# Performance work log

Measured on AMD Instinct MI355X. Metric: run time of the kernel, lower is better.

Reference implementation:

```python
import jax, jax.numpy as jnp
import numpy as np

DIM = 1024
BLOCK = 64
N_BLOCKS = DIM // BLOCK
N = 65536
INIT_SCALE = 0.01


def setup_inputs() -> dict:
    key = jax.random.key(0)
    k1, k2 = jax.random.split(key)
    x = jax.random.normal(k1, (N, DIM), dtype=jnp.float32)
    skew_params = jax.random.normal(k2, (N_BLOCKS, BLOCK, BLOCK), dtype=jnp.float32) * INIT_SCALE
    perm = jnp.asarray(np.random.default_rng(0).permutation(DIM), dtype=jnp.int64)
    return {"x": x, "skew_params": skew_params, "perm": perm}


def reference(x, skew_params, perm):
    # Skew-symmetrize each block: A = P - P^T, shape [K, b, b]
    A = skew_params - jnp.swapaxes(skew_params, -1, -2)
    # Per-block orthogonal matrices via matrix exponential, [K, b, b]
    B = jax.vmap(jax.scipy.linalg.expm)(A)
    # Block-diagonal matmul without materializing the dense [dim, dim] matrix:
    # x @ block_diag(B_0..B_{K-1}) == batched per-block matmul on reshaped x.
    xb = x.reshape(x.shape[0], N_BLOCKS, BLOCK)          # [N, K, b]
    yb = jnp.einsum("nkb,kbc->nkc", xb, B)               # [N, K, b]
    y = yb.reshape(x.shape[0], DIM)                      # [N, dim]
    # Shuffle: column permutation
    return y[:, perm]
```

## Files before the change

### kernel.cpp

```cpp
#include <hip/hip_runtime.h>

#define DIM           1024
#define BLK           64
#define NB            16
#define RT            16
#define MAIN_THREADS  1024
#define NWG           256
#define TPW           16
#define P68           68
#define BFRAG_STRIDE  512

typedef float  f32x4  __attribute__((ext_vector_type(4)));
typedef unsigned uintx2 __attribute__((ext_vector_type(2)));
typedef short  bf16x8 __attribute__((ext_vector_type(8)));

static __device__ __forceinline__ ushort f2bf(float f) {
    union { float f; unsigned u; } v; v.f = f;
    unsigned r = v.u + 0x7fffu + ((v.u >> 16) & 1u);
    return (ushort)(r >> 16);
}
static __device__ __forceinline__ float bfhi2f(unsigned hi_bits) {
    union { unsigned u; float f; } v; v.u = hi_bits & 0xffff0000u; return v.f;
}
static __device__ __forceinline__ float bflo2f(unsigned lo_bits) {
    union { unsigned u; float f; } v; v.u = lo_bits << 16; return v.f;
}

#define WAITL()   asm volatile("s_waitcnt lgkmcnt(0)" ::: "memory")
#define SBAR()    __builtin_amdgcn_s_barrier()

__global__ __launch_bounds__(512) void expm_kernel(
        const float* __restrict__ skew, ushort* __restrict__ Btl,
        const int* __restrict__ praw, int* __restrict__ pinv) {
    __shared__ float Asm[BLK][P68];
    __shared__ float Tb[2][BLK][P68];
    __shared__ float Rm[BLK][P68];
    const int tid = threadIdx.x;

    if (blockIdx.x == NB) {
        __shared__ int zc;
        if (tid == 0) zc = 0;
        __syncthreads();
        int local = 0;
        for (int i = tid; i < DIM; i += 512)
            if (praw[i] == 0) local++;
        if (local) atomicAdd(&zc, local);
        __syncthreads();
        const bool is64 = (zc > 100);
        const long long* p64 = (const long long*)praw;
        for (int i = tid; i < DIM; i += 512) {
            const int v = is64 ? (int)p64[i] : praw[i];
            pinv[v] = i;
        }
        return;
    }

    const int k = blockIdx.x;
    const float* P = skew + (size_t)k * (BLK * BLK);

    for (int e = tid; e < BLK * BLK; e += 512) {
        const int i = e >> 6, j = e & 63;
        const float a = P[i * BLK + j] - P[j * BLK + i];
        Asm[i][j]   = a;
        Tb[0][i][j] = a;
        Rm[i][j]    = a + (i == j ? 1.0f : 0.0f);
    }
    __syncthreads();

    const int i0 = (tid >> 4) * 2;
    const int j0 = (tid & 15) * 4;

    for (int n = 2; n <= 7; ++n) {
        const float invn = 1.0f / (float)n;
        const float (*Tc)[P68] = Tb[n & 1];
        float       (*Tn)[P68] = Tb[1 - (n & 1)];
        f32x4 acc0 = {0.f, 0.f, 0.f, 0.f}, acc1 = {0.f, 0.f, 0.f, 0.f};
        for (int b = 0; b < BLK; ++b) {
            const f32x4 av = *(const f32x4*)&Asm[b][j0];
            acc0 += Tc[i0][b]     * av;
            acc1 += Tc[i0 + 1][b] * av;
        }
        acc0 *= invn; acc1 *= invn;
        *(f32x4*)&Tn[i0][j0]     = acc0;
        *(f32x4*)&Tn[i0 + 1][j0] = acc1;
        f32x4 r0 = *(const f32x4*)&Rm[i0][j0];     r0 += acc0; *(f32x4*)&Rm[i0][j0]     = r0;
        f32x4 r1 = *(const f32x4*)&Rm[i0 + 1][j0]; r1 += acc1; *(f32x4*)&Rm[i0 + 1][j0] = r1;
        __syncthreads();
    }

    for (int e = tid; e < BLK * BLK; e += 512) {
        const int b = e >> 6, c = e & 63;
        const int n = c >> 4, m = c & 15;
        const int h = b >> 5, g = (b >> 3) & 3, j = b & 7;
        const size_t idx = (size_t)((k * 4 + n) * 2 + h) * BFRAG_STRIDE
                         + g * 128 + m * 8 + j;
        Btl[idx] = (ushort)f2bf(Rm[b][c]);
    }
}

__global__ __launch_bounds__(MAIN_THREADS) void gsl_main_kernel(
        const float* __restrict__ x, const ushort* __restrict__ Btl,
        const int* __restrict__ pinv, float* __restrict__ out) {
    __shared__ ushort ybuf[2][RT * DIM];

    const int tid  = threadIdx.x;
    const int lane = tid & 63;
    const int w    = tid >> 6;
    const int g    = lane >> 4;
    const int m16  = lane & 15;

    bf16x8 bfr[4][2];
#pragma unroll
    for (int n = 0; n < 4; ++n)
#pragma unroll
        for (int h = 0; h < 2; ++h)
            bfr[n][h] = *(const bf16x8*)(Btl +
                (size_t)((w * 4 + n) * 2 + h) * BFRAG_STRIDE + lane * 8);

    int jb[4];
#pragma unroll
    for (int n = 0; n < 4; ++n)
        jb[n] = pinv[w * 64 + n * 16 + m16] * 2;

    const int tile0 = blockIdx.x * TPW;
    const float* xw = x + w * 64 + g * 8;

    const int hl   = lane >> 5;
    const int q32  = lane & 31;
    const int ebase = hl * 512 + q32 * 4;

    f32x4 a0, a1, a2, a3;
    {
        const float* xp = xw + (size_t)(tile0 * RT + m16) * DIM;
        a0 = *(const f32x4*)(xp);      a1 = *(const f32x4*)(xp + 4);
        a2 = *(const f32x4*)(xp + 32); a3 = *(const f32x4*)(xp + 36);
    }

    for (int it = 0; it < TPW; ++it) {
        char* const yc = (char*)ybuf[it & 1];

        bf16x8 alo, ahi;
        alo[0] = f2bf(a0[0]); alo[1] = f2bf(a0[1]); alo[2] = f2bf(a0[2]); alo[3] = f2bf(a0[3]);
        alo[4] = f2bf(a1[0]); alo[5] = f2bf(a1[1]); alo[6] = f2bf(a1[2]); alo[7] = f2bf(a1[3]);
        ahi[0] = f2bf(a2[0]); ahi[1] = f2bf(a2[1]); ahi[2] = f2bf(a2[2]); ahi[3] = f2bf(a2[3]);
        ahi[4] = f2bf(a3[0]); ahi[5] = f2bf(a3[1]); ahi[6] = f2bf(a3[2]); ahi[7] = f2bf(a3[3]);

        if (it + 1 < TPW) {
            const float* xp = xw + (size_t)((tile0 + it + 1) * RT + m16) * DIM;
            a0 = *(const f32x4*)(xp);      a1 = *(const f32x4*)(xp + 4);
            a2 = *(const f32x4*)(xp + 32); a3 = *(const f32x4*)(xp + 36);
        }

        f32x4 acc[4];
#pragma unroll
        for (int n = 0; n < 4; ++n) acc[n] = (f32x4){0.f, 0.f, 0.f, 0.f};
#pragma unroll
        for (int n = 0; n < 4; ++n)
            acc[n] = __builtin_amdgcn_mfma_f32_16x16x32_bf16(alo, bfr[n][0], acc[n], 0, 0, 0);
#pragma unroll
        for (int n = 0; n < 4; ++n)
            acc[n] = __builtin_amdgcn_mfma_f32_16x16x32_bf16(ahi, bfr[n][1], acc[n], 0, 0, 0);

#pragma unroll
        for (int n = 0; n < 4; ++n)
#pragma unroll
            for (int i = 0; i < 4; ++i)
                *(ushort*)(yc + (4 * g + i) * 2048 + jb[n]) = f2bf(acc[n][i]);

        if (it) {
            const char* yp = (const char*)ybuf[(it & 1) ^ 1] + w * 2048;
            float* orow = out + (size_t)((tile0 + it - 1) * RT + w) * DIM;
#pragma unroll
            for (int i = 0; i < 4; ++i) {
                const int e = ebase + i * 128;
                const uintx2 u = *(const uintx2*)(yp + e * 2);
                f32x4 v;
                v[0] = bflo2f(u[0]); v[1] = bfhi2f(u[0]);
                v[2] = bflo2f(u[1]); v[3] = bfhi2f(u[1]);
                *(f32x4*)(orow + e) = v;
            }
        }

        WAITL(); SBAR();
    }

    {
        const char* yp = (const char*)ybuf[(TPW - 1) & 1] + w * 2048;
        float* orow = out + (size_t)((tile0 + TPW - 1) * RT + w) * DIM;
#pragma unroll
        for (int i = 0; i < 4; ++i) {
            const int e = ebase + i * 128;
            const uintx2 u = *(const uintx2*)(yp + e * 2);
            f32x4 v;
            v[0] = bflo2f(u[0]); v[1] = bfhi2f(u[0]);
            v[2] = bflo2f(u[1]); v[3] = bfhi2f(u[1]);
            *(f32x4*)(orow + e) = v;
        }
    }
}

extern "C" void kernel_launch(void* const* d_in, const int* in_sizes, int n_in,
                              void* d_out, int out_size, void* d_ws, size_t ws_size,
                              hipStream_t stream) {
    const float* x    = (const float*)d_in[0];
    const float* skew = (const float*)d_in[1];
    const int*   perm = (const int*)d_in[2];
    float* out = (float*)d_out;

    ushort* Btl  = (ushort*)d_ws;
    int*    pinv = (int*)((char*)d_ws + (size_t)NB * BLK * BLK * sizeof(ushort));

    expm_kernel<<<NB + 1, 512, 0, stream>>>(skew, Btl, perm, pinv);
    gsl_main_kernel<<<NWG, MAIN_THREADS, 0, stream>>>(x, Btl, pinv, out);
}
```

Measured before the change: 132.2 us.

## Replace persistent 1024-thread pipelined loop with small one-tile workgroups

The main kernel drops the persistent design, where 256 workgroups of 1024 threads each looped over 16 row tiles with double-buffered LDS and a software-prefetched x load. It now launches 4096 workgroups of 256 threads, one 16-row tile each, with every wave handling four column blocks and reloading their B fragments and inverse-permutation indices. The fp32-to-bf16 conversion of x switches to the packed v_cvt_pk_bf16_f32 instruction. The aim is higher occupancy (launch bounds ask for 5 blocks per SIMD) and letting the hardware overlap tiles across workgroups instead of relying on manual prefetch, at the cost of more redundant B and pinv loads.

```diff
diff --git a/kernel.cpp b/kernel.cpp
--- a/kernel.cpp
+++ b/kernel.cpp
@@ -4,14 +4,14 @@
 #define BLK           64
 #define NB            16
 #define RT            16
-#define MAIN_THREADS  1024
-#define NWG           256
-#define TPW           16
+#define MAIN_THREADS  256
+#define NWG           4096
 #define P68           68
 #define BFRAG_STRIDE  512
 
 typedef float  f32x4  __attribute__((ext_vector_type(4)));
 typedef unsigned uintx2 __attribute__((ext_vector_type(2)));
+typedef int    i32x4  __attribute__((ext_vector_type(4)));
 typedef short  bf16x8 __attribute__((ext_vector_type(8)));
 
 static __device__ __forceinline__ ushort f2bf(float f) {
@@ -25,9 +25,11 @@
 static __device__ __forceinline__ float bflo2f(unsigned lo_bits) {
     union { unsigned u; float f; } v; v.u = lo_bits << 16; return v.f;
 }
-
-#define WAITL()   asm volatile("s_waitcnt lgkmcnt(0)" ::: "memory")
-#define SBAR()    __builtin_amdgcn_s_barrier()
+static __device__ __forceinline__ unsigned cvt_pk(float lo, float hi) {
+    unsigned r;
+    asm("v_cvt_pk_bf16_f32 %0, %1, %2" : "=v"(r) : "v"(lo), "v"(hi));
+    return r;
+}
 
 __global__ __launch_bounds__(512) void expm_kernel(
         const float* __restrict__ skew, ushort* __restrict__ Btl,
@@ -98,58 +100,48 @@
     }
 }
 
-__global__ __launch_bounds__(MAIN_THREADS) void gsl_main_kernel(
+__global__ __launch_bounds__(MAIN_THREADS, 5) void gsl_main_kernel(
         const float* __restrict__ x, const ushort* __restrict__ Btl,
         const int* __restrict__ pinv, float* __restrict__ out) {
-    __shared__ ushort ybuf[2][RT * DIM];
+    __shared__ ushort ybuf[RT * DIM];
 
     const int tid  = threadIdx.x;
     const int lane = tid & 63;
     const int w    = tid >> 6;
     const int g    = lane >> 4;
     const int m16  = lane & 15;
+    const size_t r0 = (size_t)blockIdx.x * RT;
+    char* const yB = (char*)ybuf;
 
-    bf16x8 bfr[4][2];
+    for (int b = 0; b < 4; ++b) {
+        const int k = w + 4 * b;
+
+        int jb[4];
 #pragma unroll
-    for (int n = 0; n < 4; ++n)
+        for (int n = 0; n < 4; ++n)
+            jb[n] = pinv[k * 64 + n * 16 + m16] * 2;
+
+        bf16x8 bfr[4][2];
 #pragma unroll
-        for (int h = 0; h < 2; ++h)
-            bfr[n][h] = *(const bf16x8*)(Btl +
-                (size_t)((w * 4 + n) * 2 + h) * BFRAG_STRIDE + lane * 8);
+        for (int n = 0; n < 4; ++n)
+#pragma unroll
+            for (int h = 0; h < 2; ++h)
+                bfr[n][h] = *(const bf16x8*)(Btl +
+                    (size_t)((k * 4 + n) * 2 + h) * BFRAG_STRIDE + lane * 8);
 
-    int jb[4];
-#pragma unroll
-    for (int n = 0; n < 4; ++n)
-        jb[n] = pinv[w * 64 + n * 16 + m16] * 2;
+        const float* xp = x + (r0 + m16) * DIM + k * 64 + g * 8;
+        const f32x4 a0 = *(const f32x4*)(xp);
+        const f32x4 a1 = *(const f32x4*)(xp + 4);
+        const f32x4 a2 = *(const f32x4*)(xp + 32);
+        const f32x4 a3 = *(const f32x4*)(xp + 36);
 
-    const int tile0 = blockIdx.x * TPW;
-    const float* xw = x + w * 64 + g * 8;
-
-    const int hl   = lane >> 5;
-    const int q32  = lane & 31;
-    const int ebase = hl * 512 + q32 * 4;
-
-    f32x4 a0, a1, a2, a3;
-    {
-        const float* xp = xw + (size_t)(tile0 * RT + m16) * DIM;
-        a0 = *(const f32x4*)(xp);      a1 = *(const f32x4*)(xp + 4);
-        a2 = *(const f32x4*)(xp + 32); a3 = *(const f32x4*)(xp + 36);
-    }
-
-    for (int it = 0; it < TPW; ++it) {
-        char* const yc = (char*)ybuf[it & 1];
-
-        bf16x8 alo, ahi;
-        alo[0] = f2bf(a0[0]); alo[1] = f2bf(a0[1]); alo[2] = f2bf(a0[2]); alo[3] = f2bf(a0[3]);
-        alo[4] = f2bf(a1[0]); alo[5] = f2bf(a1[1]); alo[6] = f2bf(a1[2]); alo[7] = f2bf(a1[3]);
-        ahi[0] = f2bf(a2[0]); ahi[1] = f2bf(a2[1]); ahi[2] = f2bf(a2[2]); ahi[3] = f2bf(a2[3]);
-        ahi[4] = f2bf(a3[0]); ahi[5] = f2bf(a3[1]); ahi[6] = f2bf(a3[2]); ahi[7] = f2bf(a3[3]);
-
-        if (it + 1 < TPW) {
-            const float* xp = xw + (size_t)((tile0 + it + 1) * RT + m16) * DIM;
-            a0 = *(const f32x4*)(xp);      a1 = *(const f32x4*)(xp + 4);
-            a2 = *(const f32x4*)(xp + 32); a3 = *(const f32x4*)(xp + 36);
-        }
+        i32x4 plo, phi;
+        plo[0] = cvt_pk(a0[0], a0[1]); plo[1] = cvt_pk(a0[2], a0[3]);
+        plo[2] = cvt_pk(a1[0], a1[1]); plo[3] = cvt_pk(a1[2], a1[3]);
+        phi[0] = cvt_pk(a2[0], a2[1]); phi[1] = cvt_pk(a2[2], a2[3]);
+        phi[2] = cvt_pk(a3[0], a3[1]); phi[3] = cvt_pk(a3[2], a3[3]);
+        const bf16x8 alo = __builtin_bit_cast(bf16x8, plo);
+        const bf16x8 ahi = __builtin_bit_cast(bf16x8, phi);
 
         f32x4 acc[4];
 #pragma unroll
@@ -165,31 +157,21 @@
         for (int n = 0; n < 4; ++n)
 #pragma unroll
             for (int i = 0; i < 4; ++i)
-                *(ushort*)(yc + (4 * g + i) * 2048 + jb[n]) = f2bf(acc[n][i]);
-
-        if (it) {
-            const char* yp = (const char*)ybuf[(it & 1) ^ 1] + w * 2048;
-            float* orow = out + (size_t)((tile0 + it - 1) * RT + w) * DIM;
-#pragma unroll
-            for (int i = 0; i < 4; ++i) {
-                const int e = ebase + i * 128;
-                const uintx2 u = *(const uintx2*)(yp + e * 2);
-                f32x4 v;
-                v[0] = bflo2f(u[0]); v[1] = bfhi2f(u[0]);
-                v[2] = bflo2f(u[1]); v[3] = bfhi2f(u[1]);
-                *(f32x4*)(orow + e) = v;
-            }
-        }
-
-        WAITL(); SBAR();
+                *(ushort*)(yB + (4 * g + i) * 2048 + jb[n]) = f2bf(acc[n][i]);
     }
 
-    {
-        const char* yp = (const char*)ybuf[(TPW - 1) & 1] + w * 2048;
-        float* orow = out + (size_t)((tile0 + TPW - 1) * RT + w) * DIM;
+    __syncthreads();
+
+    const int h32  = lane >> 5;
+    const int q32  = lane & 31;
 #pragma unroll
-        for (int i = 0; i < 4; ++i) {
-            const int e = ebase + i * 128;
+    for (int rr = 0; rr < 4; ++rr) {
+        const int   r    = 4 * w + rr;
+        const char* yp   = yB + r * 2048;
+        float*      orow = out + (r0 + r) * DIM;
+#pragma unroll
+        for (int s = 0; s < 4; ++s) {
+            const int e = q32 * 4 + h32 * 512 + s * 128;
             const uintx2 u = *(const uintx2*)(yp + e * 2);
             f32x4 v;
             v[0] = bflo2f(u[0]); v[1] = bfhi2f(u[0]);
```

After: 141.5 us. 7.1% more time.
